# Performance work log

Measured on AMD Instinct MI355X. Metric: run time of the kernel, lower is better.

## Reference

```python
import jax, jax.numpy as jnp
import numpy as np

N_NODES = 50000
N_EDGES = 1250000
VOCAB = 50000
EMBED = 64
HIDDEN = 64
NUM_REL = 3
N_CLASSES = 2
N_GRAPHS = 512


def setup_inputs() -> dict:
    key = jax.random.key(0)
    ks = jax.random.split(key, 12)
    x = jax.random.randint(ks[0], (N_NODES,), 0, VOCAB, dtype=jnp.int32)
    edge_index = jax.random.randint(ks[1], (2, N_EDGES), 0, N_NODES, dtype=jnp.int32)
    edge_type = jax.random.randint(ks[2], (N_EDGES,), 0, NUM_REL, dtype=jnp.int32)
    batch = jnp.sort(jax.random.randint(ks[3], (N_NODES,), 0, N_GRAPHS, dtype=jnp.int32))
    s = 0.05
    emb = jax.random.normal(ks[4], (VOCAB, EMBED), jnp.float32) * s
    w1_rel = jax.random.normal(ks[5], (NUM_REL, EMBED, HIDDEN), jnp.float32) * s
    w1_root = jax.random.normal(ks[6], (EMBED, HIDDEN), jnp.float32) * s
    b1 = jnp.zeros((HIDDEN,), jnp.float32)
    w2_rel = jax.random.normal(ks[7], (NUM_REL, HIDDEN, HIDDEN), jnp.float32) * s
    w2_root = jax.random.normal(ks[8], (HIDDEN, HIDDEN), jnp.float32) * s
    b2 = jnp.zeros((HIDDEN,), jnp.float32)
    lin_w = jax.random.normal(ks[9], (HIDDEN, N_CLASSES), jnp.float32) * s
    lin_b = jnp.zeros((N_CLASSES,), jnp.float32)
    return {"x": x, "edge_index": edge_index, "edge_type": edge_type, "batch": batch,
            "emb": emb, "w1_rel": w1_rel, "w1_root": w1_root, "b1": b1,
            "w2_rel": w2_rel, "w2_root": w2_root, "b2": b2,
            "lin_w": lin_w, "lin_b": lin_b}


def rgcn_conv(h, src, dst, edge_type, w_rel, w_root, bias):
    # PyG RGCNConv: out = h @ W_root + bias + sum_r mean-aggregated (h_src @ W_r)
    out = h @ w_root + bias
    h_src = h[src]  # [E, F] gather
    for r in range(NUM_REL):
        mask = (edge_type == r).astype(h.dtype)  # [E]
        m = (h_src @ w_rel[r]) * mask[:, None]   # [E, H]
        s = jax.ops.segment_sum(m, dst, num_segments=N_NODES)
        cnt = jax.ops.segment_sum(mask, dst, num_segments=N_NODES)
        out = out + s / jnp.maximum(cnt, 1.0)[:, None]
    return out


def reference(x, edge_index, edge_type, batch, emb, w1_rel, w1_root, b1,
              w2_rel, w2_root, b2, lin_w, lin_b):
    src, dst = edge_index[0], edge_index[1]
    emb_eff = emb.at[0].set(0.0)  # padding_idx=0
    h = emb_eff[x]  # [N, EMBED]
    h = jax.nn.relu(rgcn_conv(h, src, dst, edge_type, w1_rel, w1_root, b1))
    h = jax.nn.relu(rgcn_conv(h, src, dst, edge_type, w2_rel, w2_root, b2))
    # global mean pool over graphs
    sums = jax.ops.segment_sum(h, batch, num_segments=N_GRAPHS)
    cnt = jax.ops.segment_sum(jnp.ones((h.shape[0],), h.dtype), batch, num_segments=N_GRAPHS)
    pooled = sums / jnp.maximum(cnt, 1.0)[:, None]  # [G, HIDDEN]
    return pooled @ lin_w + lin_b  # [G, N_CLASSES]
```

## Files before the change

kernel.cpp:

```cpp
#include <hip/hip_runtime.h>

#define CHUNK 2048

__global__ __launch_bounds__(256) void embed_count_kernel(
    const int* __restrict__ x, const float* __restrict__ emb, float* __restrict__ h0,
    const int* __restrict__ ei, int* __restrict__ pcount,
    const int* __restrict__ batch, const float* __restrict__ linb,
    float* __restrict__ inv_cnt, float* __restrict__ outg,
    int n_nodes, int n_edges, int n_bkt, int n_chk, int n_graphs,
    int embed_blocks)
{
    __shared__ int cnt[512];
    int t = threadIdx.x;
    if ((int)blockIdx.x < embed_blocks) {
        int tt = blockIdx.x * 256 + t;
        if (tt < n_nodes * 16) {
            int n = tt >> 4, q = tt & 15;
            int xv = x[n];
            float4 v = {0.f, 0.f, 0.f, 0.f};
            if (xv != 0) v = *(const float4*)(emb + (size_t)xv * 64 + q * 4);
            *(float4*)(h0 + (size_t)n * 64 + q * 4) = v;
        }
        return;
    }
    if ((int)blockIdx.x >= embed_blocks + n_chk) {
        int g = (blockIdx.x - embed_blocks - n_chk) * 256 + t;
        if (g < n_graphs) {
            int lo = 0, hi = n_nodes;
            while (lo < hi) { int mid = (lo + hi) >> 1; if (batch[mid] < g) lo = mid + 1; else hi = mid; }
            int s = lo;
            lo = 0; hi = n_nodes;
            while (lo < hi) { int mid = (lo + hi) >> 1; if (batch[mid] < g + 1) lo = mid + 1; else hi = mid; }
            inv_cnt[g] = 1.f / (float)max(lo - s, 1);
            outg[2 * g + 0] = linb[0];
            outg[2 * g + 1] = linb[1];
        }
        return;
    }
    int jb = blockIdx.x - embed_blocks;
    for (int b = t; b < 512; b += 256) cnt[b] = 0;
    __syncthreads();
    int base = jb * CHUNK;
#pragma unroll
    for (int i = 0; i < CHUNK / 256; ++i) {
        int e = base + i * 256 + t;
        if (e < n_edges) atomicAdd(&cnt[ei[n_edges + e] >> 7], 1);
    }
    __syncthreads();
    for (int b = t; b < n_bkt; b += 256) pcount[b * n_chk + jb] = cnt[b];
}

__global__ __launch_bounds__(256) void colscan_kernel(
    const int* __restrict__ pcount, int* __restrict__ pre,
    int* __restrict__ totals, int* __restrict__ rowstartR,
    int n_chk, int n_bkt, int n_edges, int n_nodes)
{
    __shared__ int ps[256];
    int b = blockIdx.x, t = threadIdx.x;
    if (b == 0 && t == 0) rowstartR[4 * n_nodes] = n_edges;
    int v[4], s = 0;
#pragma unroll
    for (int i = 0; i < 4; ++i) {
        int jj = t * 4 + i;
        v[i] = (jj < n_chk) ? pcount[b * n_chk + jj] : 0;
        s += v[i];
    }
    ps[t] = s;
    __syncthreads();
    for (int o = 1; o < 256; o <<= 1) {
        int u = (t >= o) ? ps[t - o] : 0;
        __syncthreads();
        ps[t] += u;
        __syncthreads();
    }
    int run = (t > 0) ? ps[t - 1] : 0;
#pragma unroll
    for (int i = 0; i < 4; ++i) {
        int jj = t * 4 + i;
        if (jj < n_chk) pre[jj * n_bkt + b] = run;
        run += v[i];
    }
    if (t == 255) totals[b] = run;
}

__global__ __launch_bounds__(256) void scatter_kernel(
    const int* __restrict__ ei, const int* __restrict__ et,
    const int* __restrict__ pre, const int* __restrict__ totals,
    int* __restrict__ esort, int* __restrict__ bucket_start,
    int n_edges, int n_bkt)
{
    __shared__ int bs[512], fill2[512], ps[256];
    int t = threadIdx.x, j = blockIdx.x;
    int a0 = (2 * t < n_bkt) ? totals[2 * t] : 0;
    int a1 = (2 * t + 1 < n_bkt) ? totals[2 * t + 1] : 0;
    ps[t] = a0 + a1;
    __syncthreads();
    for (int o = 1; o < 256; o <<= 1) {
        int u = (t >= o) ? ps[t - o] : 0;
        __syncthreads();
        ps[t] += u;
        __syncthreads();
    }
    int basex = (t > 0) ? ps[t - 1] : 0;
    bs[2 * t] = basex;
    bs[2 * t + 1] = basex + a0;
    fill2[t] = 0; fill2[t + 256] = 0;
    __syncthreads();
    if (j == 0) {
        for (int b = t; b < n_bkt; b += 256) bucket_start[b] = bs[b];
        if (t == 0) bucket_start[n_bkt] = n_edges;
    }
    for (int b = t; b < n_bkt; b += 256) bs[b] += pre[j * n_bkt + b];
    __syncthreads();
    int base = j * CHUNK;
#pragma unroll
    for (int i = 0; i < CHUNK / 256; ++i) {
        int e = base + i * 256 + t;
        if (e < n_edges) {
            int s = ei[e], d = ei[n_edges + e], r = et[e];
            int b = d >> 7;
            int pos = bs[b] + atomicAdd(&fill2[b], 1);
            esort[pos] = s | (r << 16) | ((d & 127) << 18);
        }
    }
}

__global__ __launch_bounds__(256) void bucket_sort_kernel(
    const int* __restrict__ bucket_start, const int* __restrict__ esort_in,
    int* __restrict__ esort_out, int* __restrict__ rowstartR, int n_nodes)
{
    __shared__ int cnt[512], off[512], fill[512], ps[256];
    int t = threadIdx.x, b = blockIdx.x;
    int s = bucket_start[b], e = bucket_start[b + 1];
    cnt[t] = 0; cnt[t + 256] = 0; fill[t] = 0; fill[t + 256] = 0;
    __syncthreads();
    for (int i = s + t; i < e; i += 256)
        atomicAdd(&cnt[(esort_in[i] >> 16) & 0x1FF], 1);
    __syncthreads();
    int a0 = cnt[2 * t], a1 = cnt[2 * t + 1];
    ps[t] = a0 + a1;
    __syncthreads();
    for (int o = 1; o < 256; o <<= 1) {
        int v = (t >= o) ? ps[t - o] : 0;
        __syncthreads();
        ps[t] += v;
        __syncthreads();
    }
    int basex = (t > 0) ? ps[t - 1] : 0;
    off[2 * t] = basex;
    off[2 * t + 1] = basex + a0;
    __syncthreads();
    int d0 = b * 128 + (2 * t >> 2);
    if (d0 < n_nodes) rowstartR[b * 512 + 2 * t] = s + off[2 * t];
    int d1 = b * 128 + ((2 * t + 1) >> 2);
    if (d1 < n_nodes) rowstartR[b * 512 + 2 * t + 1] = s + off[2 * t + 1];
    __syncthreads();
    for (int i = s + t; i < e; i += 256) {
        int p = esort_in[i];
        int bin = (p >> 16) & 0x1FF;
        int pos = s + off[bin] + atomicAdd(&fill[bin], 1);
        esort_out[pos] = p;
    }
}

__global__ __launch_bounds__(256) void agg_kernel(
    const float* __restrict__ hin, const int* __restrict__ rowstartR,
    const int* __restrict__ esort, float* __restrict__ means, int n_nodes)
{
    int wid = (blockIdx.x * 256 + threadIdx.x) >> 6;
    int lane = threadIdx.x & 63;
    if (wid >= n_nodes) return;
    int q = lane >> 4;
    int c = lane & 15;
    int4 rs = *(const int4*)(rowstartR + wid * 4);
    int s = rs.x, e = rs.w;

    float4 a0 = {0.f,0.f,0.f,0.f}, a1 = {0.f,0.f,0.f,0.f}, a2 = {0.f,0.f,0.f,0.f};

    int i = s + 4 * q;
    for (; i + 4 <= e; i += 16) {
        int p0 = esort[i], p1 = esort[i + 1], p2 = esort[i + 2], p3 = esort[i + 3];
        float4 v0 = *(const float4*)(hin + (size_t)(p0 & 0xFFFF) * 64 + c * 4);
        float4 v1 = *(const float4*)(hin + (size_t)(p1 & 0xFFFF) * 64 + c * 4);
        float4 v2 = *(const float4*)(hin + (size_t)(p2 & 0xFFFF) * 64 + c * 4);
        float4 v3 = *(const float4*)(hin + (size_t)(p3 & 0xFFFF) * 64 + c * 4);
#pragma unroll
        for (int m = 0; m < 4; ++m) {
            int p = m == 0 ? p0 : m == 1 ? p1 : m == 2 ? p2 : p3;
            float4 v = m == 0 ? v0 : m == 1 ? v1 : m == 2 ? v2 : v3;
            int r = (p >> 16) & 3;
            float m0 = (r == 0) ? 1.f : 0.f;
            float m1 = (r == 1) ? 1.f : 0.f;
            float m2 = (r == 2) ? 1.f : 0.f;
            a0.x = fmaf(m0, v.x, a0.x); a0.y = fmaf(m0, v.y, a0.y);
            a0.z = fmaf(m0, v.z, a0.z); a0.w = fmaf(m0, v.w, a0.w);
            a1.x = fmaf(m1, v.x, a1.x); a1.y = fmaf(m1, v.y, a1.y);
            a1.z = fmaf(m1, v.z, a1.z); a1.w = fmaf(m1, v.w, a1.w);
            a2.x = fmaf(m2, v.x, a2.x); a2.y = fmaf(m2, v.y, a2.y);
            a2.z = fmaf(m2, v.z, a2.z); a2.w = fmaf(m2, v.w, a2.w);
        }
    }
#pragma unroll
    for (int m = 0; m < 3; ++m) {
        int ii = i + m;
        if (ii < e) {
            int p = esort[ii];
            float4 v = *(const float4*)(hin + (size_t)(p & 0xFFFF) * 64 + c * 4);
            int r = (p >> 16) & 3;
            float m0 = (r == 0) ? 1.f : 0.f;
            float m1 = (r == 1) ? 1.f : 0.f;
            float m2 = (r == 2) ? 1.f : 0.f;
            a0.x = fmaf(m0, v.x, a0.x); a0.y = fmaf(m0, v.y, a0.y);
            a0.z = fmaf(m0, v.z, a0.z); a0.w = fmaf(m0, v.w, a0.w);
            a1.x = fmaf(m1, v.x, a1.x); a1.y = fmaf(m1, v.y, a1.y);
            a1.z = fmaf(m1, v.z, a1.z); a1.w = fmaf(m1, v.w, a1.w);
            a2.x = fmaf(m2, v.x, a2.x); a2.y = fmaf(m2, v.y, a2.y);
            a2.z = fmaf(m2, v.z, a2.z); a2.w = fmaf(m2, v.w, a2.w);
        }
    }
#pragma unroll
    for (int off = 16; off < 64; off <<= 1) {
        a0.x += __shfl_xor(a0.x, off); a0.y += __shfl_xor(a0.y, off);
        a0.z += __shfl_xor(a0.z, off); a0.w += __shfl_xor(a0.w, off);
        a1.x += __shfl_xor(a1.x, off); a1.y += __shfl_xor(a1.y, off);
        a1.z += __shfl_xor(a1.z, off); a1.w += __shfl_xor(a1.w, off);
        a2.x += __shfl_xor(a2.x, off); a2.y += __shfl_xor(a2.y, off);
        a2.z += __shfl_xor(a2.z, off); a2.w += __shfl_xor(a2.w, off);
    }
    if (q < 3) {
        int cnt = (q == 0) ? (rs.y - rs.x) : (q == 1) ? (rs.z - rs.y) : (rs.w - rs.z);
        float4 a = (q == 0) ? a0 : (q == 1) ? a1 : a2;
        float inv = 1.f / (float)max(cnt, 1);
        float4 m = {a.x * inv, a.y * inv, a.z * inv, a.w * inv};
        *(float4*)(means + (size_t)wid * 192 + q * 64 + c * 4) = m;
    }
}

__global__ __launch_bounds__(256, 4) void transform_kernel(
    const float* __restrict__ hin, const float* __restrict__ means,
    const float* __restrict__ wroot, const float* __restrict__ wrel,
    const float* __restrict__ bias, float* __restrict__ hout,
    const int* __restrict__ batch, const float* __restrict__ linw,
    const float* __restrict__ inv_cnt, float* __restrict__ outg,
    int n_nodes, int do_pool)
{
    __shared__ float smem[2][64 * 68];
    int t = threadIdx.x;
    int lane = t & 63;
    int wv = __builtin_amdgcn_readfirstlane(t >> 6);
    int j0 = wv * 16;
    int n0g = blockIdx.x * 64;

    int sn_ = t >> 4;
    int sk  = (t & 15) * 4;

    float4 stg[4];
#pragma unroll
    for (int r = 0; r < 4; ++r) {
        int node = r * 16 + sn_;
        int gn = min(n0g + node, n_nodes - 1);
        stg[r] = *(const float4*)(hin + (size_t)gn * 64 + sk);
    }
#pragma unroll
    for (int r = 0; r < 4; ++r) {
        int node = r * 16 + sn_;
        *(float4*)&smem[0][node * 68 + sk] = stg[r];
    }

    float acc[16];
#pragma unroll
    for (int i = 0; i < 16; ++i) acc[i] = bias[j0 + i];
    __syncthreads();

    for (int p = 0; p < 4; ++p) {
        if (p < 3) {
#pragma unroll
            for (int r = 0; r < 4; ++r) {
                int node = r * 16 + sn_;
                int gn = min(n0g + node, n_nodes - 1);
                stg[r] = *(const float4*)(means + (size_t)gn * 192 + p * 64 + sk);
            }
        }
        const float* wb = ((p == 0) ? wroot : (wrel + (size_t)(p - 1) * 4096)) + j0;
        const float* lv = &smem[p & 1][lane * 68];
#pragma unroll 4
        for (int k4 = 0; k4 < 16; ++k4) {
            float4 v = *(const float4*)(lv + k4 * 4);
#pragma unroll
            for (int kk = 0; kk < 4; ++kk) {
                float vk = kk == 0 ? v.x : kk == 1 ? v.y : kk == 2 ? v.z : v.w;
                const float* wr = wb + (k4 * 4 + kk) * 64;
#pragma unroll
                for (int i = 0; i < 16; ++i)
                    acc[i] = fmaf(vk, wr[i], acc[i]);
            }
        }
        if (p < 3) {
            __syncthreads();
#pragma unroll
            for (int r = 0; r < 4; ++r) {
                int node = r * 16 + sn_;
                *(float4*)&smem[(p + 1) & 1][node * 68 + sk] = stg[r];
            }
            __syncthreads();
        }
    }

    if (!do_pool) {
        __syncthreads();
        float* osh = smem[0];
#pragma unroll
        for (int i4 = 0; i4 < 4; ++i4) {
            float4 r;
            r.x = fmaxf(acc[i4 * 4 + 0], 0.f);
            r.y = fmaxf(acc[i4 * 4 + 1], 0.f);
            r.z = fmaxf(acc[i4 * 4 + 2], 0.f);
            r.w = fmaxf(acc[i4 * 4 + 3], 0.f);
            *(float4*)&osh[lane * 68 + j0 + i4 * 4] = r;
        }
        __syncthreads();
#pragma unroll
        for (int r = 0; r < 4; ++r) {
            int node = r * 16 + sn_;
            int gn = n0g + node;
            if (gn < n_nodes)
                *(float4*)(hout + (size_t)gn * 64 + sk) =
                    *(const float4*)&osh[node * 68 + sk];
        }
    } else {
        float d0 = 0.f, d1 = 0.f;
#pragma unroll
        for (int i = 0; i < 16; ++i) {
            float rr = fmaxf(acc[i], 0.f);
            d0 = fmaf(rr, linw[(j0 + i) * 2 + 0], d0);
            d1 = fmaf(rr, linw[(j0 + i) * 2 + 1], d1);
        }
        __syncthreads();
        float* wsum = smem[0];
        float* gacc = smem[0] + 512;
        wsum[(wv * 64 + lane) * 2 + 0] = d0;
        wsum[(wv * 64 + lane) * 2 + 1] = d1;
        if (t < 128) gacc[t] = 0.f;
        __syncthreads();
        int gmin = batch[min(n0g, n_nodes - 1)];
        if (t < 64) {
            int gn = n0g + t;
            if (gn < n_nodes) {
                float s0 = wsum[t * 2]     + wsum[128 + t * 2] +
                           wsum[256 + t * 2] + wsum[384 + t * 2];
                float s1 = wsum[t * 2 + 1]     + wsum[128 + t * 2 + 1] +
                           wsum[256 + t * 2 + 1] + wsum[384 + t * 2 + 1];
                int gg = batch[gn];
                float ic = inv_cnt[gg];
                int idx = gg - gmin;
                if (idx < 64) {
                    atomicAdd(&gacc[idx * 2 + 0], s0 * ic);
                    atomicAdd(&gacc[idx * 2 + 1], s1 * ic);
                } else {
                    atomicAdd(&outg[2 * gg + 0], s0 * ic);
                    atomicAdd(&outg[2 * gg + 1], s1 * ic);
                }
            }
        }
        __syncthreads();
        if (t < 64) {
            float v0 = gacc[t * 2], v1 = gacc[t * 2 + 1];
            if (v0 != 0.f || v1 != 0.f) {
                atomicAdd(&outg[2 * (gmin + t) + 0], v0);
                atomicAdd(&outg[2 * (gmin + t) + 1], v1);
            }
        }
    }
}

extern "C" void kernel_launch(void* const* d_in, const int* in_sizes, int n_in,
                              void* d_out, int out_size, void* d_ws, size_t ws_size,
                              hipStream_t stream)
{
    const int*   x      = (const int*)d_in[0];
    const int*   ei     = (const int*)d_in[1];
    const int*   et     = (const int*)d_in[2];
    const int*   batch  = (const int*)d_in[3];
    const float* emb    = (const float*)d_in[4];
    const float* w1rel  = (const float*)d_in[5];
    const float* w1root = (const float*)d_in[6];
    const float* b1     = (const float*)d_in[7];
    const float* w2rel  = (const float*)d_in[8];
    const float* w2root = (const float*)d_in[9];
    const float* b2     = (const float*)d_in[10];
    const float* linw   = (const float*)d_in[11];
    const float* linb   = (const float*)d_in[12];
    float* out = (float*)d_out;

    const int N = in_sizes[0];
    const int E = in_sizes[2];
    const int G = out_size / 2;
    const int NBKT = (N + 127) >> 7;
    const int NCHK = (E + CHUNK - 1) / CHUNK;

    float* hA        = (float*)d_ws;
    float* hB        = hA + (size_t)N * 64;
    float* means     = hB + (size_t)N * 64;
    int*   esort     = (int*)(means + (size_t)N * 192);
    int*   rowstartR = esort + E;
    int*   bucket_start = rowstartR + 4 * N + 4;
    int*   totals    = bucket_start + NBKT + 1;
    float* inv_cnt   = (float*)(totals + NBKT);
    int*   esort2    = (int*)(inv_cnt + G);
    int*   pcount    = (int*)means + 4 * 1024 * 1024;
    int*   pre       = (int*)means + 5 * 1024 * 1024;

    int embedBlocks = (N * 16 + 255) / 256;
    int gBlocks = (G + 255) / 256;
    embed_count_kernel<<<embedBlocks + NCHK + gBlocks, 256, 0, stream>>>(
        x, emb, hA, ei, pcount, batch, linb, inv_cnt, out,
        N, E, NBKT, NCHK, G, embedBlocks);
    colscan_kernel<<<NBKT, 256, 0, stream>>>(
        pcount, pre, totals, rowstartR, NCHK, NBKT, E, N);
    scatter_kernel<<<NCHK, 256, 0, stream>>>(ei, et, pre, totals, esort, bucket_start, E, NBKT);
    bucket_sort_kernel<<<NBKT, 256, 0, stream>>>(bucket_start, esort, esort2, rowstartR, N);

    int aggBlocks = (N * 64 + 255) / 256;
    int tfBlocks  = (N + 63) / 64;
    agg_kernel<<<aggBlocks, 256, 0, stream>>>(hA, rowstartR, esort2, means, N);
    transform_kernel<<<tfBlocks, 256, 0, stream>>>(
        hA, means, w1root, w1rel, b1, hB, batch, linw, inv_cnt, out, N, 0);
    agg_kernel<<<aggBlocks, 256, 0, stream>>>(hB, rowstartR, esort2, means, N);
    transform_kernel<<<tfBlocks, 256, 0, stream>>>(
        hB, means, w2root, w2rel, b2, hA, batch, linw, inv_cnt, out, N, 1);
}
```

Measured before the change: 298.7 us.

## Replace two-level bucket sort with direct global-atomic counting sort per (dst, relation)

Edges are now counted with global atomics into per-(destination, relation) bins. A two-stage block scan then produces row starts directly, and a single scatter pass uses global atomic fill counters. This replaces the per-chunk histogram, the column scan and the second in-bucket sort pass, along with the intermediate esort buffer. In exchange it issues many contended global atomics twice and adds a memset, and the edge order within each bin becomes nondeterministic.

```diff
diff --git a/kernel.cpp b/kernel.cpp
--- a/kernel.cpp
+++ b/kernel.cpp
@@ -4,13 +4,12 @@
 
 __global__ __launch_bounds__(256) void embed_count_kernel(
     const int* __restrict__ x, const float* __restrict__ emb, float* __restrict__ h0,
-    const int* __restrict__ ei, int* __restrict__ pcount,
+    const int* __restrict__ ei, const int* __restrict__ et,
+    int* __restrict__ cnt4,
     const int* __restrict__ batch, const float* __restrict__ linb,
     float* __restrict__ inv_cnt, float* __restrict__ outg,
-    int n_nodes, int n_edges, int n_bkt, int n_chk, int n_graphs,
-    int embed_blocks)
-{
-    __shared__ int cnt[512];
+    int n_nodes, int n_edges, int n_chk, int n_graphs, int embed_blocks)
+{
     int t = threadIdx.x;
     if ((int)blockIdx.x < embed_blocks) {
         int tt = blockIdx.x * 256 + t;
@@ -38,31 +37,28 @@
         return;
     }
     int jb = blockIdx.x - embed_blocks;
-    for (int b = t; b < 512; b += 256) cnt[b] = 0;
-    __syncthreads();
     int base = jb * CHUNK;
 #pragma unroll
     for (int i = 0; i < CHUNK / 256; ++i) {
         int e = base + i * 256 + t;
-        if (e < n_edges) atomicAdd(&cnt[ei[n_edges + e] >> 7], 1);
-    }
-    __syncthreads();
-    for (int b = t; b < n_bkt; b += 256) pcount[b * n_chk + jb] = cnt[b];
-}
-
-__global__ __launch_bounds__(256) void colscan_kernel(
-    const int* __restrict__ pcount, int* __restrict__ pre,
-    int* __restrict__ totals, int* __restrict__ rowstartR,
-    int n_chk, int n_bkt, int n_edges, int n_nodes)
+        if (e < n_edges) {
+            int d = ei[n_edges + e], r = et[e];
+            atomicAdd(&cnt4[d * 4 + r], 1);
+        }
+    }
+}
+
+__global__ __launch_bounds__(256) void scan1_kernel(
+    const int* __restrict__ cnt4, int* __restrict__ rs4,
+    int* __restrict__ bsum, int n_bins)
 {
     __shared__ int ps[256];
     int b = blockIdx.x, t = threadIdx.x;
-    if (b == 0 && t == 0) rowstartR[4 * n_nodes] = n_edges;
+    int base = b * 1024 + t * 4;
     int v[4], s = 0;
 #pragma unroll
     for (int i = 0; i < 4; ++i) {
-        int jj = t * 4 + i;
-        v[i] = (jj < n_chk) ? pcount[b * n_chk + jj] : 0;
+        v[i] = (base + i < n_bins) ? cnt4[base + i] : 0;
         s += v[i];
     }
     ps[t] = s;
@@ -76,24 +72,19 @@
     int run = (t > 0) ? ps[t - 1] : 0;
 #pragma unroll
     for (int i = 0; i < 4; ++i) {
-        int jj = t * 4 + i;
-        if (jj < n_chk) pre[jj * n_bkt + b] = run;
+        if (base + i < n_bins) rs4[base + i] = run;
         run += v[i];
     }
-    if (t == 255) totals[b] = run;
-}
-
-__global__ __launch_bounds__(256) void scatter_kernel(
-    const int* __restrict__ ei, const int* __restrict__ et,
-    const int* __restrict__ pre, const int* __restrict__ totals,
-    int* __restrict__ esort, int* __restrict__ bucket_start,
-    int n_edges, int n_bkt)
-{
-    __shared__ int bs[512], fill2[512], ps[256];
-    int t = threadIdx.x, j = blockIdx.x;
-    int a0 = (2 * t < n_bkt) ? totals[2 * t] : 0;
-    int a1 = (2 * t + 1 < n_bkt) ? totals[2 * t + 1] : 0;
-    ps[t] = a0 + a1;
+    if (t == 255) bsum[b] = run;
+}
+
+__global__ __launch_bounds__(256) void scan2_kernel(
+    const int* __restrict__ bsum, int* __restrict__ boff, int nb)
+{
+    __shared__ int ps[256];
+    int t = threadIdx.x;
+    int v = (t < nb) ? bsum[t] : 0;
+    ps[t] = v;
     __syncthreads();
     for (int o = 1; o < 256; o <<= 1) {
         int u = (t >= o) ? ps[t - o] : 0;
@@ -101,71 +92,32 @@
         ps[t] += u;
         __syncthreads();
     }
-    int basex = (t > 0) ? ps[t - 1] : 0;
-    bs[2 * t] = basex;
-    bs[2 * t + 1] = basex + a0;
-    fill2[t] = 0; fill2[t + 256] = 0;
-    __syncthreads();
-    if (j == 0) {
-        for (int b = t; b < n_bkt; b += 256) bucket_start[b] = bs[b];
-        if (t == 0) bucket_start[n_bkt] = n_edges;
-    }
-    for (int b = t; b < n_bkt; b += 256) bs[b] += pre[j * n_bkt + b];
-    __syncthreads();
-    int base = j * CHUNK;
+    if (t < nb) boff[t] = ps[t] - v;
+}
+
+__global__ __launch_bounds__(256) void scatter_kernel(
+    const int* __restrict__ ei, const int* __restrict__ et,
+    const int* __restrict__ rs4, const int* __restrict__ boff,
+    int* __restrict__ fill4, int* __restrict__ esort, int n_edges)
+{
+    int t = threadIdx.x;
+    int base = blockIdx.x * CHUNK;
 #pragma unroll
     for (int i = 0; i < CHUNK / 256; ++i) {
         int e = base + i * 256 + t;
         if (e < n_edges) {
             int s = ei[e], d = ei[n_edges + e], r = et[e];
-            int b = d >> 7;
-            int pos = bs[b] + atomicAdd(&fill2[b], 1);
-            esort[pos] = s | (r << 16) | ((d & 127) << 18);
-        }
-    }
-}
-
-__global__ __launch_bounds__(256) void bucket_sort_kernel(
-    const int* __restrict__ bucket_start, const int* __restrict__ esort_in,
-    int* __restrict__ esort_out, int* __restrict__ rowstartR, int n_nodes)
-{
-    __shared__ int cnt[512], off[512], fill[512], ps[256];
-    int t = threadIdx.x, b = blockIdx.x;
-    int s = bucket_start[b], e = bucket_start[b + 1];
-    cnt[t] = 0; cnt[t + 256] = 0; fill[t] = 0; fill[t + 256] = 0;
-    __syncthreads();
-    for (int i = s + t; i < e; i += 256)
-        atomicAdd(&cnt[(esort_in[i] >> 16) & 0x1FF], 1);
-    __syncthreads();
-    int a0 = cnt[2 * t], a1 = cnt[2 * t + 1];
-    ps[t] = a0 + a1;
-    __syncthreads();
-    for (int o = 1; o < 256; o <<= 1) {
-        int v = (t >= o) ? ps[t - o] : 0;
-        __syncthreads();
-        ps[t] += v;
-        __syncthreads();
-    }
-    int basex = (t > 0) ? ps[t - 1] : 0;
-    off[2 * t] = basex;
-    off[2 * t + 1] = basex + a0;
-    __syncthreads();
-    int d0 = b * 128 + (2 * t >> 2);
-    if (d0 < n_nodes) rowstartR[b * 512 + 2 * t] = s + off[2 * t];
-    int d1 = b * 128 + ((2 * t + 1) >> 2);
-    if (d1 < n_nodes) rowstartR[b * 512 + 2 * t + 1] = s + off[2 * t + 1];
-    __syncthreads();
-    for (int i = s + t; i < e; i += 256) {
-        int p = esort_in[i];
-        int bin = (p >> 16) & 0x1FF;
-        int pos = s + off[bin] + atomicAdd(&fill[bin], 1);
-        esort_out[pos] = p;
+            int bin = d * 4 + r;
+            int pos = rs4[bin] + boff[bin >> 10] + atomicAdd(&fill4[bin], 1);
+            esort[pos] = s | (r << 16);
+        }
     }
 }
 
 __global__ __launch_bounds__(256) void agg_kernel(
     const float* __restrict__ hin, const int* __restrict__ rowstartR,
-    const int* __restrict__ esort, float* __restrict__ means, int n_nodes)
+    const int* __restrict__ boff, const int* __restrict__ esort,
+    float* __restrict__ means, int n_nodes)
 {
     int wid = (blockIdx.x * 256 + threadIdx.x) >> 6;
     int lane = threadIdx.x & 63;
@@ -173,6 +125,8 @@
     int q = lane >> 4;
     int c = lane & 15;
     int4 rs = *(const int4*)(rowstartR + wid * 4);
+    int off = boff[(wid * 4) >> 10];
+    rs.x += off; rs.y += off; rs.z += off; rs.w += off;
     int s = rs.x, e = rs.w;
 
     float4 a0 = {0.f,0.f,0.f,0.f}, a1 = {0.f,0.f,0.f,0.f}, a2 = {0.f,0.f,0.f,0.f};
@@ -219,13 +173,13 @@
         }
     }
 #pragma unroll
-    for (int off = 16; off < 64; off <<= 1) {
-        a0.x += __shfl_xor(a0.x, off); a0.y += __shfl_xor(a0.y, off);
-        a0.z += __shfl_xor(a0.z, off); a0.w += __shfl_xor(a0.w, off);
-        a1.x += __shfl_xor(a1.x, off); a1.y += __shfl_xor(a1.y, off);
-        a1.z += __shfl_xor(a1.z, off); a1.w += __shfl_xor(a1.w, off);
-        a2.x += __shfl_xor(a2.x, off); a2.y += __shfl_xor(a2.y, off);
-        a2.z += __shfl_xor(a2.z, off); a2.w += __shfl_xor(a2.w, off);
+    for (int off2 = 16; off2 < 64; off2 <<= 1) {
+        a0.x += __shfl_xor(a0.x, off2); a0.y += __shfl_xor(a0.y, off2);
+        a0.z += __shfl_xor(a0.z, off2); a0.w += __shfl_xor(a0.w, off2);
+        a1.x += __shfl_xor(a1.x, off2); a1.y += __shfl_xor(a1.y, off2);
+        a1.z += __shfl_xor(a1.z, off2); a1.w += __shfl_xor(a1.w, off2);
+        a2.x += __shfl_xor(a2.x, off2); a2.y += __shfl_xor(a2.y, off2);
+        a2.z += __shfl_xor(a2.z, off2); a2.w += __shfl_xor(a2.w, off2);
     }
     if (q < 3) {
         int cnt = (q == 0) ? (rs.y - rs.x) : (q == 1) ? (rs.z - rs.y) : (rs.w - rs.z);
@@ -395,37 +349,38 @@
     const int N = in_sizes[0];
     const int E = in_sizes[2];
     const int G = out_size / 2;
-    const int NBKT = (N + 127) >> 7;
     const int NCHK = (E + CHUNK - 1) / CHUNK;
+    const int NBINS = 4 * N;
+    const int SBLK = (NBINS + 1023) / 1024;
 
     float* hA        = (float*)d_ws;
     float* hB        = hA + (size_t)N * 64;
     float* means     = hB + (size_t)N * 64;
     int*   esort     = (int*)(means + (size_t)N * 192);
     int*   rowstartR = esort + E;
-    int*   bucket_start = rowstartR + 4 * N + 4;
-    int*   totals    = bucket_start + NBKT + 1;
-    float* inv_cnt   = (float*)(totals + NBKT);
-    int*   esort2    = (int*)(inv_cnt + G);
-    int*   pcount    = (int*)means + 4 * 1024 * 1024;
-    int*   pre       = (int*)means + 5 * 1024 * 1024;
+    float* inv_cnt   = (float*)(rowstartR + 4 * N + 4);
+    int*   bsum      = (int*)(inv_cnt + G);
+    int*   boff      = bsum + 256;
+    int*   cnt4      = (int*)means;
+    int*   fill4     = cnt4 + NBINS;
+
+    hipMemsetAsync(cnt4, 0, (size_t)2 * NBINS * sizeof(int), stream);
 
     int embedBlocks = (N * 16 + 255) / 256;
     int gBlocks = (G + 255) / 256;
     embed_count_kernel<<<embedBlocks + NCHK + gBlocks, 256, 0, stream>>>(
-        x, emb, hA, ei, pcount, batch, linb, inv_cnt, out,
-        N, E, NBKT, NCHK, G, embedBlocks);
-    colscan_kernel<<<NBKT, 256, 0, stream>>>(
-        pcount, pre, totals, rowstartR, NCHK, NBKT, E, N);
-    scatter_kernel<<<NCHK, 256, 0, stream>>>(ei, et, pre, totals, esort, bucket_start, E, NBKT);
-    bucket_sort_kernel<<<NBKT, 256, 0, stream>>>(bucket_start, esort, esort2, rowstartR, N);
+        x, emb, hA, ei, et, cnt4, batch, linb, inv_cnt, out,
+        N, E, NCHK, G, embedBlocks);
+    scan1_kernel<<<SBLK, 256, 0, stream>>>(cnt4, rowstartR, bsum, NBINS);
+    scan2_kernel<<<1, 256, 0, stream>>>(bsum, boff, SBLK);
+    scatter_kernel<<<NCHK, 256, 0, stream>>>(ei, et, rowstartR, boff, fill4, esort, E);
 
     int aggBlocks = (N * 64 + 255) / 256;
     int tfBlocks  = (N + 63) / 64;
-    agg_kernel<<<aggBlocks, 256, 0, stream>>>(hA, rowstartR, esort2, means, N);
+    agg_kernel<<<aggBlocks, 256, 0, stream>>>(hA, rowstartR, boff, esort, means, N);
     transform_kernel<<<tfBlocks, 256, 0, stream>>>(
         hA, means, w1root, w1rel, b1, hB, batch, linw, inv_cnt, out, N, 0);
-    agg_kernel<<<aggBlocks, 256, 0, stream>>>(hB, rowstartR, esort2, means, N);
+    agg_kernel<<<aggBlocks, 256, 0, stream>>>(hB, rowstartR, boff, esort, means, N);
     transform_kernel<<<tfBlocks, 256, 0, stream>>>(
         hB, means, w2root, w2rel, b2, hA, batch, linw, inv_cnt, out, N, 1);
 }
```

New measurement: 380.9 us. +27.5%, slower.
